# Optimization experiments

Hardware: AMD Instinct MI355X
Metric: run time of the kernel (lower is better)

## Reference

```python
import jax, jax.numpy as jnp
import numpy as np


def setup_inputs() -> dict:
    key = jax.random.key(0)
    k1, k2, k3, k4 = jax.random.split(key, 4)
    B, T, C, H = 16, 2048, 1024, 128
    x = jax.random.normal(k1, (B, T, C), dtype=jnp.float32)
    # bias-free Dense kernels (stored as [in, out] like keras)
    s = 1.0 / np.sqrt(C)
    Wk = jax.random.normal(k2, (C, H), dtype=jnp.float32) * s
    Wq = jax.random.normal(k3, (C, H), dtype=jnp.float32) * s
    Wv = jax.random.normal(k4, (C, H), dtype=jnp.float32) * s
    return {"x": x, "Wk": Wk, "Wq": Wq, "Wv": Wv}


def reference(x, Wk, Wq, Wv):
    # single-head causal self-attention (dropout inactive at inference)
    B, T, C = x.shape
    H = Wk.shape[-1]
    k = jnp.einsum('btc,ch->bth', x, Wk)   # [B,T,H]
    q = jnp.einsum('btc,ch->bth', x, Wq)
    v = jnp.einsum('btc,ch->bth', x, Wv)
    scale = 1.0 / jnp.sqrt(jnp.float32(H))
    wei = jnp.einsum('bqh,bkh->bqk', q, k) * scale          # [B,T,T]
    causal = jnp.tril(jnp.ones((T, T), dtype=bool))
    wei = jnp.where(causal, wei, -jnp.inf)
    wei = jax.nn.softmax(wei, axis=-1)
    out = jnp.einsum('bqk,bkh->bqh', wei, v)                # [B,T,H]
    return out
```

## Files before the change

### kernel.cpp

```cpp
#include <hip/hip_runtime.h>
#include <hip/hip_bf16.h>

typedef __bf16 bf16x8_t __attribute__((ext_vector_type(8)));
typedef __bf16 bf16x4_t __attribute__((ext_vector_type(4)));
typedef float  f32x4_t  __attribute__((ext_vector_type(4)));

#define MFMA_16x16x32_BF16(A, B, C) __builtin_amdgcn_mfma_f32_16x16x32_bf16((A), (B), (C), 0, 0, 0)

static constexpr int B_ = 16;
static constexpr int T_ = 2048;
static constexpr int C_ = 1024;
static constexpr int H_ = 128;
static constexpr long M_ = (long)B_ * T_;

__global__ __launch_bounds__(128) void wt_kernel(
    const float* __restrict__ Wq, const float* __restrict__ Wk,
    const float* __restrict__ Wv, __bf16* __restrict__ WT)
{
    const int z = blockIdx.y;
    const float* __restrict__ W = (z == 0) ? Wq : (z == 1) ? Wk : Wv;
    const int h  = threadIdx.x;
    const int c0 = blockIdx.x * 8;
    bf16x8_t v;
    #pragma unroll
    for (int j = 0; j < 8; ++j)
        v[j] = (__bf16)W[(c0 + j) * H_ + h];
    *(bf16x8_t*)&WT[((long)z * H_ + h) * C_ + c0] = v;
}

__global__ __launch_bounds__(256) void proj_kernel(
    const float*  __restrict__ x,
    const __bf16* __restrict__ WT,
    __bf16* __restrict__ qo,
    __bf16* __restrict__ ko,
    __bf16* __restrict__ vo)
{
    __shared__ __bf16 XS[64 * 40];
    __shared__ __bf16 WS[384 * 40];

    const int tid  = threadIdx.x;
    const int lane = tid & 63;
    const int w    = tid >> 6;
    const int m16  = lane & 15;
    const int quad = lane >> 4;
    const int koff = quad * 8;

    const long r0 = (long)blockIdx.x * 64;

    f32x4_t acc[24];
    #pragma unroll
    for (int nt = 0; nt < 24; ++nt) acc[nt] = f32x4_t{0, 0, 0, 0};

    for (int k0 = 0; k0 < C_; k0 += 32) {
        #pragma unroll
        for (int ch = 0; ch < 2; ++ch) {
            int s   = tid + 256 * ch;
            int row = s >> 3, c = s & 7;
            f32x4_t xv = *(const f32x4_t*)&x[(r0 + row) * C_ + k0 + c * 4];
            bf16x4_t xb;
            #pragma unroll
            for (int j = 0; j < 4; ++j) xb[j] = (__bf16)xv[j];
            *(bf16x4_t*)&XS[row * 40 + c * 4] = xb;
        }
        #pragma unroll
        for (int ch = 0; ch < 6; ++ch) {
            int g = tid + 256 * ch;
            int n = g >> 2, kc = g & 3;
            *(bf16x8_t*)&WS[n * 40 + kc * 8] =
                *(const bf16x8_t*)&WT[(long)n * C_ + k0 + kc * 8];
        }
        __syncthreads();

        bf16x8_t a = *(const bf16x8_t*)&XS[(w * 16 + m16) * 40 + koff];
        #pragma unroll
        for (int nt = 0; nt < 24; ++nt) {
            bf16x8_t bfr = *(const bf16x8_t*)&WS[(nt * 16 + m16) * 40 + koff];
            acc[nt] = MFMA_16x16x32_BF16(a, bfr, acc[nt]);
        }
        __syncthreads();
    }

    const long rbase = r0 + w * 16 + quad * 4;
    #pragma unroll
    for (int nt = 0; nt < 24; ++nt) {
        int z = nt >> 3;
        int h = (nt & 7) * 16 + m16;
        if (z < 2) {
            __bf16* __restrict__ o = z ? ko : qo;
            #pragma unroll
            for (int r = 0; r < 4; ++r)
                o[(rbase + r) * H_ + h] = (__bf16)acc[nt][r];
        } else {
            long bb = rbase >> 11, tt = rbase & 2047;
            bf16x4_t pk;
            #pragma unroll
            for (int r = 0; r < 4; ++r) pk[r] = (__bf16)acc[nt][r];
            *(bf16x4_t*)&vo[bb * (H_ * (long)T_) + h * (long)T_ + tt] = pk;
        }
    }
}

__global__ __launch_bounds__(256) void attn_kernel(
    const __bf16* __restrict__ q,
    const __bf16* __restrict__ k,
    const __bf16* __restrict__ vT,
    float* __restrict__ out)
{
    __shared__ __bf16 KS[64 * 136];
    __shared__ __bf16 VS[128 * 72];
    __shared__ __bf16 PS[4][16 * 72];

    const int L   = blockIdx.x;
    const int b   = L & 15;
    const int Lh  = L >> 4;
    const int qb  = (Lh < 16) ? (31 - Lh) : (Lh - 16);

    const int tid  = threadIdx.x;
    const int w    = tid >> 6;
    const int lane = tid & 63;
    const int m16  = lane & 15;
    const int quad = lane >> 4;
    const int koff = quad * 8;

    const __bf16* __restrict__ qp = q  + (long)b * T_ * H_;
    const __bf16* __restrict__ kp = k  + (long)b * T_ * H_;
    const __bf16* __restrict__ vp = vT + (long)b * H_ * T_;

    const int q0w = qb * 64 + w * 16;
    const int qg  = q0w + m16;

    bf16x8_t qfr[4];
    #pragma unroll
    for (int s = 0; s < 4; ++s)
        qfr[s] = *(const bf16x8_t*)&qp[(q0w + m16) * H_ + s * 32 + koff];

    f32x4_t acc[8];
    #pragma unroll
    for (int i = 0; i < 8; ++i) acc[i] = f32x4_t{0, 0, 0, 0};
    float mrun = -1e30f, lrun = 0.f;

    __bf16* Pb = &PS[w][0];
    const float SC = 0.08838834764831845f;
    const int kend = qb * 64 + 64;

    const int krow = tid >> 4, kc16 = tid & 15;
    const int vrow = tid >> 3, vc8  = tid & 7;

    for (int tk0 = 0; tk0 < kend; tk0 += 64) {
        __syncthreads();
        #pragma unroll
        for (int ch = 0; ch < 4; ++ch) {
            int r = krow + ch * 16;
            *(bf16x8_t*)&KS[r * 136 + kc16 * 8] =
                *(const bf16x8_t*)&kp[(tk0 + r) * H_ + kc16 * 8];
        }
        #pragma unroll
        for (int ch = 0; ch < 4; ++ch) {
            int hh = vrow + ch * 32;
            *(bf16x8_t*)&VS[hh * 72 + vc8 * 8] =
                *(const bf16x8_t*)&vp[hh * (long)T_ + tk0 + vc8 * 8];
        }
        __syncthreads();

        f32x4_t st[4];
        #pragma unroll
        for (int kt = 0; kt < 4; ++kt) {
            f32x4_t s = f32x4_t{0, 0, 0, 0};
            #pragma unroll
            for (int sI = 0; sI < 4; ++sI) {
                bf16x8_t kf = *(const bf16x8_t*)&KS[(kt * 16 + m16) * 136 + sI * 32 + koff];
                s = MFMA_16x16x32_BF16(kf, qfr[sI], s);
            }
            st[kt] = s;
        }

        float vv[4][4];
        if (tk0 + 63 <= q0w) {
            #pragma unroll
            for (int kt = 0; kt < 4; ++kt)
                #pragma unroll
                for (int r = 0; r < 4; ++r)
                    vv[kt][r] = st[kt][r] * SC;
        } else {
            #pragma unroll
            for (int kt = 0; kt < 4; ++kt)
                #pragma unroll
                for (int r = 0; r < 4; ++r) {
                    int kg = tk0 + kt * 16 + quad * 4 + r;
                    vv[kt][r] = (kg <= qg) ? st[kt][r] * SC : -1e30f;
                }
        }

        float mloc = -1e30f;
        #pragma unroll
        for (int kt = 0; kt < 4; ++kt)
            #pragma unroll
            for (int r = 0; r < 4; ++r)
                mloc = fmaxf(mloc, vv[kt][r]);
        mloc = fmaxf(mloc, __shfl_xor(mloc, 16, 64));
        mloc = fmaxf(mloc, __shfl_xor(mloc, 32, 64));

        float mnew = fmaxf(mrun, mloc);
        float al   = __expf(mrun - mnew);
        float psum = 0.f;
        #pragma unroll
        for (int kt = 0; kt < 4; ++kt) {
            bf16x4_t pk;
            #pragma unroll
            for (int r = 0; r < 4; ++r) {
                float p = __expf(vv[kt][r] - mnew);
                psum += p;
                pk[r] = (__bf16)p;
            }
            *(bf16x4_t*)&Pb[m16 * 72 + kt * 16 + quad * 4] = pk;
        }
        psum += __shfl_xor(psum, 16, 64);
        psum += __shfl_xor(psum, 32, 64);
        mrun = mnew;
        lrun = lrun * al + psum;

        #pragma unroll
        for (int i = 0; i < 8; ++i)
            #pragma unroll
            for (int r = 0; r < 4; ++r)
                acc[i][r] *= al;

        #pragma unroll
        for (int half = 0; half < 2; ++half) {
            bf16x8_t pa = *(const bf16x8_t*)&Pb[m16 * 72 + half * 32 + koff];
            #pragma unroll
            for (int i = 0; i < 8; ++i) {
                bf16x8_t vf = *(const bf16x8_t*)&VS[(i * 16 + m16) * 72 + half * 32 + koff];
                acc[i] = MFMA_16x16x32_BF16(vf, pa, acc[i]);
            }
        }
    }

    float* __restrict__ ob = out + (long)b * T_ * H_;
    const float inv = 1.f / lrun;
    #pragma unroll
    for (int i = 0; i < 8; ++i) {
        f32x4_t o;
        #pragma unroll
        for (int r = 0; r < 4; ++r) o[r] = acc[i][r] * inv;
        *(f32x4_t*)&ob[(q0w + m16) * H_ + i * 16 + quad * 4] = o;
    }
}

extern "C" void kernel_launch(void* const* d_in, const int* in_sizes, int n_in,
                              void* d_out, int out_size, void* d_ws, size_t ws_size,
                              hipStream_t stream)
{
    const float* x  = (const float*)d_in[0];
    const float* Wk = (const float*)d_in[1];
    const float* Wq = (const float*)d_in[2];
    const float* Wv = (const float*)d_in[3];

    __bf16* qws = (__bf16*)d_ws;
    __bf16* kws = qws + M_ * H_;
    __bf16* vws = kws + M_ * H_;
    __bf16* WT  = vws + (long)B_ * H_ * T_;
    float*  out = (float*)d_out;

    wt_kernel  <<<dim3(C_ / 8, 3), 128, 0, stream>>>(Wq, Wk, Wv, WT);
    proj_kernel<<<dim3((int)(M_ / 64)), 256, 0, stream>>>(x, WT, qws, kws, vws);
    attn_kernel<<<dim3(512), 256, 0, stream>>>(qws, kws, vws, out);
}
```

Measured before the change: 275.4 us.

## Double-buffer x tiles in projection and register-prefetch K/V in attention

The projection kernel now handles 32 rows per block. Each wave owns 6 output column tiles and reads W fragments directly from global memory (L2) instead of staging all 384 columns in shared memory. The x tile is double-buffered, so the next slice loads while MFMAs run and one barrier per step is removed. The attention kernel prefetches the next K/V tile into registers before computing the current one, hiding global load latency. The trade-offs are that W reads now go uncoalesced through cache, the grid doubles, and register pressure rises.

```diff
diff --git a/kernel.cpp b/kernel.cpp
--- a/kernel.cpp
+++ b/kernel.cpp
@@ -35,8 +35,7 @@
     __bf16* __restrict__ ko,
     __bf16* __restrict__ vo)
 {
-    __shared__ __bf16 XS[64 * 40];
-    __shared__ __bf16 WS[384 * 40];
+    __shared__ __bf16 XS[2][32 * 40];
 
     const int tid  = threadIdx.x;
     const int lane = tid & 63;
@@ -45,57 +44,73 @@
     const int quad = lane >> 4;
     const int koff = quad * 8;
 
-    const long r0 = (long)blockIdx.x * 64;
-
-    f32x4_t acc[24];
-    #pragma unroll
-    for (int nt = 0; nt < 24; ++nt) acc[nt] = f32x4_t{0, 0, 0, 0};
+    const long r0 = (long)blockIdx.x * 32;
+    const int xrow = tid >> 3, xc4 = tid & 7;
+
+    f32x4_t acc[2][6];
+    #pragma unroll
+    for (int mt = 0; mt < 2; ++mt)
+        #pragma unroll
+        for (int nt = 0; nt < 6; ++nt)
+            acc[mt][nt] = f32x4_t{0, 0, 0, 0};
+
+    {
+        f32x4_t xv = *(const f32x4_t*)&x[(r0 + xrow) * C_ + xc4 * 4];
+        bf16x4_t xb;
+        #pragma unroll
+        for (int j = 0; j < 4; ++j) xb[j] = (__bf16)xv[j];
+        *(bf16x4_t*)&XS[0][xrow * 40 + xc4 * 4] = xb;
+    }
+    __syncthreads();
 
     for (int k0 = 0; k0 < C_; k0 += 32) {
-        #pragma unroll
-        for (int ch = 0; ch < 2; ++ch) {
-            int s   = tid + 256 * ch;
-            int row = s >> 3, c = s & 7;
-            f32x4_t xv = *(const f32x4_t*)&x[(r0 + row) * C_ + k0 + c * 4];
+        const int par = (k0 >> 5) & 1;
+        const bool more = (k0 + 32 < C_);
+
+        f32x4_t xv;
+        if (more)
+            xv = *(const f32x4_t*)&x[(r0 + xrow) * C_ + k0 + 32 + xc4 * 4];
+
+        bf16x8_t a0 = *(const bf16x8_t*)&XS[par][m16 * 40 + koff];
+        bf16x8_t a1 = *(const bf16x8_t*)&XS[par][(16 + m16) * 40 + koff];
+
+        #pragma unroll
+        for (int nt = 0; nt < 6; ++nt) {
+            const int ntg = w * 6 + nt;
+            bf16x8_t bfr = *(const bf16x8_t*)&WT[(long)(ntg * 16 + m16) * C_ + k0 + koff];
+            acc[0][nt] = MFMA_16x16x32_BF16(a0, bfr, acc[0][nt]);
+            acc[1][nt] = MFMA_16x16x32_BF16(a1, bfr, acc[1][nt]);
+        }
+
+        if (more) {
             bf16x4_t xb;
             #pragma unroll
             for (int j = 0; j < 4; ++j) xb[j] = (__bf16)xv[j];
-            *(bf16x4_t*)&XS[row * 40 + c * 4] = xb;
-        }
-        #pragma unroll
-        for (int ch = 0; ch < 6; ++ch) {
-            int g = tid + 256 * ch;
-            int n = g >> 2, kc = g & 3;
-            *(bf16x8_t*)&WS[n * 40 + kc * 8] =
-                *(const bf16x8_t*)&WT[(long)n * C_ + k0 + kc * 8];
+            *(bf16x4_t*)&XS[par ^ 1][xrow * 40 + xc4 * 4] = xb;
         }
         __syncthreads();
-
-        bf16x8_t a = *(const bf16x8_t*)&XS[(w * 16 + m16) * 40 + koff];
-        #pragma unroll
-        for (int nt = 0; nt < 24; ++nt) {
-            bf16x8_t bfr = *(const bf16x8_t*)&WS[(nt * 16 + m16) * 40 + koff];
-            acc[nt] = MFMA_16x16x32_BF16(a, bfr, acc[nt]);
-        }
-        __syncthreads();
-    }
-
-    const long rbase = r0 + w * 16 + quad * 4;
-    #pragma unroll
-    for (int nt = 0; nt < 24; ++nt) {
-        int z = nt >> 3;
-        int h = (nt & 7) * 16 + m16;
-        if (z < 2) {
-            __bf16* __restrict__ o = z ? ko : qo;
-            #pragma unroll
-            for (int r = 0; r < 4; ++r)
-                o[(rbase + r) * H_ + h] = (__bf16)acc[nt][r];
-        } else {
-            long bb = rbase >> 11, tt = rbase & 2047;
-            bf16x4_t pk;
-            #pragma unroll
-            for (int r = 0; r < 4; ++r) pk[r] = (__bf16)acc[nt][r];
-            *(bf16x4_t*)&vo[bb * (H_ * (long)T_) + h * (long)T_ + tt] = pk;
+    }
+
+    #pragma unroll
+    for (int mt = 0; mt < 2; ++mt) {
+        const long rbase = r0 + mt * 16 + quad * 4;
+        #pragma unroll
+        for (int nt = 0; nt < 6; ++nt) {
+            const int ntg = w * 6 + nt;
+            const int z = ntg >> 3;
+            const int h = (ntg & 7) * 16 + m16;
+            if (z < 2) {
+                __bf16* __restrict__ o = z ? ko : qo;
+                #pragma unroll
+                for (int r = 0; r < 4; ++r)
+                    o[(rbase + r) * H_ + h] = (__bf16)acc[mt][nt][r];
+            } else {
+                long bb = rbase >> 11, tt = rbase & 2047;
+                bf16x4_t pk;
+                #pragma unroll
+                for (int r = 0; r < 4; ++r) pk[r] = (__bf16)acc[mt][nt][r];
+                *(bf16x4_t*)&vo[bb * (H_ * (long)T_) + h * (long)T_ + tt] = pk;
+            }
         }
     }
 }
@@ -146,21 +161,32 @@
     const int krow = tid >> 4, kc16 = tid & 15;
     const int vrow = tid >> 3, vc8  = tid & 7;
 
+    bf16x8_t kr[4], vr[4];
+    #pragma unroll
+    for (int ch = 0; ch < 4; ++ch)
+        kr[ch] = *(const bf16x8_t*)&kp[(krow + ch * 16) * H_ + kc16 * 8];
+    #pragma unroll
+    for (int ch = 0; ch < 4; ++ch)
+        vr[ch] = *(const bf16x8_t*)&vp[(vrow + ch * 32) * (long)T_ + vc8 * 8];
+
     for (int tk0 = 0; tk0 < kend; tk0 += 64) {
         __syncthreads();
         #pragma unroll
-        for (int ch = 0; ch < 4; ++ch) {
-            int r = krow + ch * 16;
-            *(bf16x8_t*)&KS[r * 136 + kc16 * 8] =
-                *(const bf16x8_t*)&kp[(tk0 + r) * H_ + kc16 * 8];
-        }
-        #pragma unroll
-        for (int ch = 0; ch < 4; ++ch) {
-            int hh = vrow + ch * 32;
-            *(bf16x8_t*)&VS[hh * 72 + vc8 * 8] =
-                *(const bf16x8_t*)&vp[hh * (long)T_ + tk0 + vc8 * 8];
-        }
+        for (int ch = 0; ch < 4; ++ch)
+            *(bf16x8_t*)&KS[(krow + ch * 16) * 136 + kc16 * 8] = kr[ch];
+        #pragma unroll
+        for (int ch = 0; ch < 4; ++ch)
+            *(bf16x8_t*)&VS[(vrow + ch * 32) * 72 + vc8 * 8] = vr[ch];
         __syncthreads();
+
+        if (tk0 + 64 < kend) {
+            #pragma unroll
+            for (int ch = 0; ch < 4; ++ch)
+                kr[ch] = *(const bf16x8_t*)&kp[(tk0 + 64 + krow + ch * 16) * H_ + kc16 * 8];
+            #pragma unroll
+            for (int ch = 0; ch < 4; ++ch)
+                vr[ch] = *(const bf16x8_t*)&vp[(vrow + ch * 32) * (long)T_ + tk0 + 64 + vc8 * 8];
+        }
 
         f32x4_t st[4];
         #pragma unroll
@@ -263,6 +289,6 @@
     float*  out = (float*)d_out;
 
     wt_kernel  <<<dim3(C_ / 8, 3), 128, 0, stream>>>(Wq, Wk, Wv, WT);
-    proj_kernel<<<dim3((int)(M_ / 64)), 256, 0, stream>>>(x, WT, qws, kws, vws);
+    proj_kernel<<<dim3((int)(M_ / 32)), 256, 0, stream>>>(x, WT, qws, kws, vws);
     attn_kernel<<<dim3(512), 256, 0, stream>>>(qws, kws, vws, out);
 }
```

Measured after the change: 338.0 us. 1.23x slower.
